# Optimization experiments

Hardware: AMD Instinct MI355X
Metric: run time of the kernel (lower is better)

The kernel has to match this reference:

```python
import jax, jax.numpy as jnp
import numpy as np

B, S, D = 2, 2048, 1024
H = 16
HD = D // H
MINUS_INFINITY = -1000000000.0


def setup_inputs() -> dict:
    key = jax.random.key(0)
    ks = jax.random.split(key, 6)
    sc = 0.02
    return {
        "x": jax.random.normal(ks[0], (B, S, D), dtype=jnp.float32),
        "Wq": jax.random.normal(ks[1], (D, D), dtype=jnp.float32) * sc,
        "Wk": jax.random.normal(ks[2], (D, D), dtype=jnp.float32) * sc,
        "Wv": jax.random.normal(ks[3], (D, D), dtype=jnp.float32) * sc,
        "Wo": jax.random.normal(ks[4], (D, D), dtype=jnp.float32) * sc,
        "bo": jnp.zeros((D,), dtype=jnp.float32),
    }


def reference(x, Wq, Wk, Wv, Wo, bo):
    b, n, _ = x.shape
    # Linear with transpose_b=True: x @ W.T
    q = jnp.einsum('bnd,ed->bne', x, Wq).reshape(b, n, H, HD).transpose(0, 2, 1, 3)
    k = jnp.einsum('bnd,ed->bne', x, Wk).reshape(b, n, H, HD).transpose(0, 2, 1, 3)
    v = jnp.einsum('bnd,ed->bne', x, Wv).reshape(b, n, H, HD).transpose(0, 2, 1, 3)
    scores = jnp.einsum('bhqd,bhkd->bhqk', q, k) * (1.0 / HD ** 0.5)
    mask = jnp.triu(jnp.ones((n, n), dtype=scores.dtype), k=1) * MINUS_INFINITY
    scores = scores + mask[None, None, :, :]
    attn = jax.nn.softmax(scores, axis=-1)  # dropout prob = 0.0
    ctx = jnp.einsum('bhqk,bhkd->bhqd', attn, v)
    ctx = ctx.transpose(0, 2, 1, 3).reshape(b, n, D)
    return jnp.einsum('bnd,ed->bne', ctx, Wo) + bo
```

## Files before the change

kernel.cpp:

```cpp
#include <hip/hip_runtime.h>
#include <hip/hip_bf16.h>

#define B_  2
#define S_  2048
#define D_  1024
#define H_  16
#define HD_ 64

typedef __attribute__((ext_vector_type(8))) short short8;
typedef __attribute__((ext_vector_type(4))) float f32x4;

__device__ __forceinline__ unsigned short f2b(float f) {
    __hip_bfloat16 h = __float2bfloat16(f);
    unsigned short u;
    __builtin_memcpy(&u, &h, 2);
    return u;
}

__device__ __forceinline__ float exp2_raw(float x) {
    float r;
    asm("v_exp_f32 %0, %1" : "=v"(r) : "v"(x));
    return r;
}

__device__ __forceinline__ unsigned int cvt_pk_bf16(float lo, float hi) {
    unsigned int r;
    asm("v_cvt_pk_bf16_f32 %0, %1, %2" : "=v"(r) : "v"(lo), "v"(hi));
    return r;
}

typedef __attribute__((address_space(1))) const unsigned int g_u32;
typedef __attribute__((address_space(3))) unsigned int l_u32;
__device__ __forceinline__ void gload_lds16(const void* g, void* l) {
    __builtin_amdgcn_global_load_lds((g_u32*)g, (l_u32*)l, 16, 0, 0);
}

__global__ __launch_bounds__(256) void convert_kernel(
    const float* __restrict__ x,  const float* __restrict__ Wq,
    const float* __restrict__ Wk, const float* __restrict__ Wv,
    const float* __restrict__ Wo, unsigned short* __restrict__ dst)
{
    const long long i4 = blockIdx.x * 256 + threadIdx.x;
    const long long e  = i4 * 4;
    const long long M1 = 1048576LL;
    const float* src;
    if      (e < 4 * M1) src = x  + e;
    else if (e < 5 * M1) src = Wq + (e - 4 * M1);
    else if (e < 6 * M1) src = Wk + (e - 5 * M1);
    else if (e < 7 * M1) src = Wv + (e - 6 * M1);
    else                 src = Wo + (e - 7 * M1);
    float4 v = *(const float4*)src;
    unsigned long long pk = (unsigned long long)f2b(v.x)
                          | ((unsigned long long)f2b(v.y) << 16)
                          | ((unsigned long long)f2b(v.z) << 32)
                          | ((unsigned long long)f2b(v.w) << 48);
    *(unsigned long long*)&dst[e] = pk;
}

__global__ __launch_bounds__(256) void qkv_proj_kernel(
    const unsigned short* __restrict__ x,
    const unsigned short* __restrict__ Wq,
    const unsigned short* __restrict__ Wk,
    const unsigned short* __restrict__ Wv,
    unsigned short* __restrict__ q_ws,
    unsigned short* __restrict__ k_ws,
    unsigned short* __restrict__ vT_ws)
{
    __shared__ unsigned short a_lds[2][128 * 32];
    __shared__ unsigned short b_lds[2][128 * 32];

    const int m0 = blockIdx.x * 128;
    const int n0 = blockIdx.y * 128;
    const int which = blockIdx.z;
    const unsigned short* W = (which == 0) ? Wq : (which == 1) ? Wk : Wv;

    const int tid  = threadIdx.x;
    const int wave = tid >> 6;
    const int lane = tid & 63;
    const int l15  = lane & 15;
    const int quad = lane >> 4;
    const int wm = (wave & 1) * 64;
    const int wn = (wave >> 1) * 64;

    const int srow = tid >> 2;
    const int scol = (tid & 3) * 8;
    const int soff = tid * 8;

    f32x4 acc[4][4];
    #pragma unroll
    for (int sm = 0; sm < 4; ++sm)
        #pragma unroll
        for (int sn = 0; sn < 4; ++sn)
            #pragma unroll
            for (int r = 0; r < 4; ++r) acc[sm][sn][r] = 0.f;

    #pragma unroll
    for (int p = 0; p < 2; ++p) {
        gload_lds16(&x[(m0 + srow + p * 64) * D_ + scol], &a_lds[0][p * 2048 + soff]);
        gload_lds16(&W[(n0 + srow + p * 64) * D_ + scol], &b_lds[0][p * 2048 + soff]);
    }
    __syncthreads();

    for (int t = 0; t < 32; ++t) {
        const int cur = t & 1;
        if (t < 31) {
            const int kk = (t + 1) * 32;
            #pragma unroll
            for (int p = 0; p < 2; ++p) {
                gload_lds16(&x[(m0 + srow + p * 64) * D_ + kk + scol],
                            &a_lds[cur ^ 1][p * 2048 + soff]);
                gload_lds16(&W[(n0 + srow + p * 64) * D_ + kk + scol],
                            &b_lds[cur ^ 1][p * 2048 + soff]);
            }
        }
        short8 af[4], bf[4];
        #pragma unroll
        for (int s = 0; s < 4; ++s) {
            af[s] = *(const short8*)&a_lds[cur][(wm + s * 16 + l15) * 32 + quad * 8];
            bf[s] = *(const short8*)&b_lds[cur][(wn + s * 16 + l15) * 32 + quad * 8];
        }
        #pragma unroll
        for (int sm = 0; sm < 4; ++sm)
            #pragma unroll
            for (int sn = 0; sn < 4; ++sn)
                acc[sm][sn] = __builtin_amdgcn_mfma_f32_16x16x32_bf16(
                    af[sm], bf[sn], acc[sm][sn], 0, 0, 0);
        __syncthreads();
    }

    #pragma unroll
    for (int sm = 0; sm < 4; ++sm) {
        #pragma unroll
        for (int sn = 0; sn < 4; ++sn) {
            const int n  = n0 + wn + sn * 16 + l15;
            const int h  = n >> 6;
            const int hd = n & 63;
            const int mbase = m0 + wm + sm * 16 + quad * 4;
            const int b     = mbase >> 11;
            const int sbase = mbase & 2047;
            if (which == 2) {
                unsigned long long pk =
                      (unsigned long long)cvt_pk_bf16(acc[sm][sn][0], acc[sm][sn][1])
                    | ((unsigned long long)cvt_pk_bf16(acc[sm][sn][2], acc[sm][sn][3]) << 32);
                *(unsigned long long*)&vT_ws[((b * H_ + h) * HD_ + hd) * S_ + sbase] = pk;
            } else if (which == 0) {
                #pragma unroll
                for (int r = 0; r < 4; ++r)
                    q_ws[((b * H_ + h) * S_ + (sbase + r)) * HD_ + hd] =
                        f2b(acc[sm][sn][r] * (0.125f * 1.44269504f));
            } else {
                #pragma unroll
                for (int r = 0; r < 4; ++r)
                    k_ws[((b * H_ + h) * S_ + (sbase + r)) * HD_ + hd] =
                        f2b(acc[sm][sn][r]);
            }
        }
    }
}

__global__ __launch_bounds__(256) void attn_kernel(
    const unsigned short* __restrict__ q_ws,
    const unsigned short* __restrict__ k_ws,
    const unsigned short* __restrict__ vT_ws,
    unsigned short* __restrict__ ctx_ws)
{
    __shared__ unsigned short k_lds[2 * 64 * 64];
    __shared__ unsigned short vT_lds[2 * 64 * 64];

    const int bh = blockIdx.x;
    const int qt = 31 - (int)blockIdx.y;

    const int tid  = threadIdx.x;
    const int wave = tid >> 6;
    const int lane = tid & 63;
    const int l15  = lane & 15;
    const int quad = lane >> 4;
    const int r0   = tid >> 3;
    const int c8   = tid & 7;

    const unsigned short* Qh = q_ws + bh * (S_ * HD_);
    const unsigned short* Kh = k_ws + bh * (S_ * HD_);
    const unsigned short* Vt = vT_ws + bh * (HD_ * S_);
    const int b = bh >> 4;
    const int h = bh & 15;

    const int src0 = l15 + 32 * (quad & 1);
    const int src1 = src0 + 16;
    const int sel  = quad >> 1;

    const int qg = qt * 64 + wave * 16 + l15;

    const int scol = (c8 ^ (r0 & 7)) * 8;
    const int d0 = r0 * 64 + c8 * 8;
    const int d1 = d0 + 2048;
    const int xr8 = (l15 & 7) << 3;

    gload_lds16(&Kh[r0 * HD_ + scol],        &k_lds[d0]);
    gload_lds16(&Kh[(r0 + 32) * HD_ + scol], &k_lds[d1]);
    gload_lds16(&Vt[r0 * S_ + scol],         &vT_lds[d0]);
    gload_lds16(&Vt[(r0 + 32) * S_ + scol],  &vT_lds[d1]);

    short8 aq[2];
    aq[0] = *(const short8*)&Qh[qg * HD_ + quad * 8];
    aq[1] = *(const short8*)&Qh[qg * HD_ + 32 + quad * 8];

    __syncthreads();

    float l_lane = 0.f;
    f32x4 o[4];
    #pragma unroll
    for (int f = 0; f < 4; ++f)
        #pragma unroll
        for (int r = 0; r < 4; ++r) o[f][r] = 0.f;

    for (int kt = 0; kt <= qt; ++kt) {
        const int cb = (kt & 1) * 4096;
        if (kt < qt) {
            const int nk0 = (kt + 1) * 64;
            const int nbb = 4096 - cb;
            gload_lds16(&Kh[(nk0 + r0) * HD_ + scol],      &k_lds[nbb + d0]);
            gload_lds16(&Kh[(nk0 + r0 + 32) * HD_ + scol], &k_lds[nbb + d1]);
            gload_lds16(&Vt[r0 * S_ + nk0 + scol],         &vT_lds[nbb + d0]);
            gload_lds16(&Vt[(r0 + 32) * S_ + nk0 + scol],  &vT_lds[nbb + d1]);
        }

        f32x4 sc[4];
        #pragma unroll
        for (int f = 0; f < 4; ++f)
            #pragma unroll
            for (int r = 0; r < 4; ++r) sc[f][r] = 0.f;
        #pragma unroll
        for (int f = 0; f < 4; ++f)
            #pragma unroll
            for (int kc = 0; kc < 2; ++kc) {
                short8 ak = *(const short8*)&k_lds[cb + (f * 16 + l15) * 64
                                                  + ((kc * 32 + quad * 8) ^ xr8)];
                sc[f] = __builtin_amdgcn_mfma_f32_16x16x32_bf16(ak, aq[kc], sc[f], 0, 0, 0);
            }

        float p[4][4];
        if (kt == qt) {
            const int kbase = kt * 64 + quad * 4;
            #pragma unroll
            for (int f = 0; f < 4; ++f)
                #pragma unroll
                for (int r = 0; r < 4; ++r) {
                    const float pv = exp2_raw(sc[f][r]);
                    p[f][r] = (kbase + f * 16 + r > qg) ? 0.f : pv;
                    l_lane += p[f][r];
                }
        } else {
            #pragma unroll
            for (int f = 0; f < 4; ++f)
                #pragma unroll
                for (int r = 0; r < 4; ++r) {
                    p[f][r] = exp2_raw(sc[f][r]);
                    l_lane += p[f][r];
                }
        }

        unsigned int pd[4][2];
        #pragma unroll
        for (int f = 0; f < 4; ++f) {
            pd[f][0] = cvt_pk_bf16(p[f][0], p[f][1]);
            pd[f][1] = cvt_pk_bf16(p[f][2], p[f][3]);
        }

        #pragma unroll
        for (int c = 0; c < 2; ++c) {
            const int a0 = __shfl((int)pd[c * 2][0],     src0, 64);
            const int a1 = __shfl((int)pd[c * 2][1],     src0, 64);
            const int a2 = __shfl((int)pd[c * 2][0],     src1, 64);
            const int a3 = __shfl((int)pd[c * 2][1],     src1, 64);
            const int b0 = __shfl((int)pd[c * 2 + 1][0], src0, 64);
            const int b1 = __shfl((int)pd[c * 2 + 1][1], src0, 64);
            const int b2 = __shfl((int)pd[c * 2 + 1][0], src1, 64);
            const int b3 = __shfl((int)pd[c * 2 + 1][1], src1, 64);
            union { int i[4]; short8 s; } u2;
            u2.i[0] = sel ? b0 : a0;
            u2.i[1] = sel ? b1 : a1;
            u2.i[2] = sel ? b2 : a2;
            u2.i[3] = sel ? b3 : a3;
            #pragma unroll
            for (int f = 0; f < 4; ++f) {
                short8 av = *(const short8*)&vT_lds[cb + (f * 16 + l15) * 64
                                                   + ((c * 32 + quad * 8) ^ xr8)];
                o[f] = __builtin_amdgcn_mfma_f32_16x16x32_bf16(av, u2.s, o[f], 0, 0, 0);
            }
        }

        __syncthreads();
    }

    float l = l_lane;
    l += __shfl_xor(l, 16, 64);
    l += __shfl_xor(l, 32, 64);
    const float inv_l = 1.0f / l;

    #pragma unroll
    for (int f = 0; f < 4; ++f) {
        unsigned long long pk =
              (unsigned long long)cvt_pk_bf16(o[f][0] * inv_l, o[f][1] * inv_l)
            | ((unsigned long long)cvt_pk_bf16(o[f][2] * inv_l, o[f][3] * inv_l) << 32);
        *(unsigned long long*)&ctx_ws[(b * S_ + qg) * D_ + h * 64 + f * 16 + quad * 4] = pk;
    }
}

__global__ __launch_bounds__(256) void out_proj_kernel(
    const unsigned short* __restrict__ ctx,
    const unsigned short* __restrict__ Wo,
    const float* __restrict__ bo,
    float* __restrict__ out)
{
    __shared__ unsigned short a_lds[2][128 * 32];
    __shared__ unsigned short b_lds[2][128 * 32];

    const int m0 = blockIdx.x * 128;
    const int n0 = blockIdx.y * 128;

    const int tid  = threadIdx.x;
    const int wave = tid >> 6;
    const int lane = tid & 63;
    const int l15  = lane & 15;
    const int quad = lane >> 4;
    const int wm = (wave & 1) * 64;
    const int wn = (wave >> 1) * 64;

    const int srow = tid >> 2;
    const int scol = (tid & 3) * 8;
    const int soff = tid * 8;

    f32x4 acc[4][4];
    #pragma unroll
    for (int sm = 0; sm < 4; ++sm)
        #pragma unroll
        for (int sn = 0; sn < 4; ++sn)
            #pragma unroll
            for (int r = 0; r < 4; ++r) acc[sm][sn][r] = 0.f;

    #pragma unroll
    for (int p = 0; p < 2; ++p) {
        gload_lds16(&ctx[(m0 + srow + p * 64) * D_ + scol], &a_lds[0][p * 2048 + soff]);
        gload_lds16(&Wo[(n0 + srow + p * 64) * D_ + scol],  &b_lds[0][p * 2048 + soff]);
    }
    __syncthreads();

    for (int t = 0; t < 32; ++t) {
        const int cur = t & 1;
        if (t < 31) {
            const int kk = (t + 1) * 32;
            #pragma unroll
            for (int p = 0; p < 2; ++p) {
                gload_lds16(&ctx[(m0 + srow + p * 64) * D_ + kk + scol],
                            &a_lds[cur ^ 1][p * 2048 + soff]);
                gload_lds16(&Wo[(n0 + srow + p * 64) * D_ + kk + scol],
                            &b_lds[cur ^ 1][p * 2048 + soff]);
            }
        }
        short8 af[4], bf[4];
        #pragma unroll
        for (int s = 0; s < 4; ++s) {
            af[s] = *(const short8*)&a_lds[cur][(wm + s * 16 + l15) * 32 + quad * 8];
            bf[s] = *(const short8*)&b_lds[cur][(wn + s * 16 + l15) * 32 + quad * 8];
        }
        #pragma unroll
        for (int sm = 0; sm < 4; ++sm)
            #pragma unroll
            for (int sn = 0; sn < 4; ++sn)
                acc[sm][sn] = __builtin_amdgcn_mfma_f32_16x16x32_bf16(
                    af[sm], bf[sn], acc[sm][sn], 0, 0, 0);
        __syncthreads();
    }

    #pragma unroll
    for (int sm = 0; sm < 4; ++sm) {
        #pragma unroll
        for (int sn = 0; sn < 4; ++sn) {
            const int n = n0 + wn + sn * 16 + l15;
            const float bias = bo[n];
            const int mbase = m0 + wm + sm * 16 + quad * 4;
            #pragma unroll
            for (int r = 0; r < 4; ++r)
                out[(mbase + r) * D_ + n] = acc[sm][sn][r] + bias;
        }
    }
}

extern "C" void kernel_launch(void* const* d_in, const int* in_sizes, int n_in,
                              void* d_out, int out_size, void* d_ws, size_t ws_size,
                              hipStream_t stream) {
    const float* x  = (const float*)d_in[0];
    const float* Wq = (const float*)d_in[1];
    const float* Wk = (const float*)d_in[2];
    const float* Wv = (const float*)d_in[3];
    const float* Wo = (const float*)d_in[4];
    const float* bo = (const float*)d_in[5];
    float* out = (float*)d_out;

    const size_t M1 = 1048576;
    const size_t SZ = 4 * M1;

    unsigned short* xb  = (unsigned short*)d_ws;
    unsigned short* wqb = xb  + SZ;
    unsigned short* wkb = wqb + M1;
    unsigned short* wvb = wkb + M1;
    unsigned short* wob = wvb + M1;
    unsigned short* q_ws   = wob + M1;
    unsigned short* k_ws   = q_ws + SZ;
    unsigned short* vT_ws  = k_ws + SZ;
    unsigned short* ctx_ws = vT_ws + SZ;

    convert_kernel<<<dim3(8192), 256, 0, stream>>>(x, Wq, Wk, Wv, Wo, xb);
    qkv_proj_kernel<<<dim3(32, 8, 3), 256, 0, stream>>>(xb, wqb, wkb, wvb, q_ws, k_ws, vT_ws);
    attn_kernel<<<dim3(32, 32), 256, 0, stream>>>(q_ws, k_ws, vT_ws, ctx_ws);
    out_proj_kernel<<<dim3(32, 8), 256, 0, stream>>>(ctx_ws, wob, bo, out);
}
```

Measured before the change: 191.6 us.

## Restructure attention into single-wave blocks reading K/V directly from global

Replaces the 4-wave, LDS double-buffered attention kernel with 2048 one-wave workgroups, each handling 32 query rows as two 16-row halves. K and V are loaded directly from global memory (relying on L2/cache) instead of being staged through LDS, and each loaded K/V fragment is reused across both query halves. The diagonal tile is specialised so the even half-tile skips unnecessary work. This removes LDS traffic and __syncthreads but gives up cross-wave sharing of K/V tiles, increasing global/L2 load volume and exposing load latency without explicit prefetch.

```diff
diff --git a/kernel.cpp b/kernel.cpp
--- a/kernel.cpp
+++ b/kernel.cpp
@@ -158,25 +158,115 @@
     }
 }
 
-__global__ __launch_bounds__(256) void attn_kernel(
+template<int FMAX, int CMAX, bool MASK>
+__device__ __forceinline__ void attn_tile(
+    const int k0,
+    const unsigned short* __restrict__ Kh,
+    const unsigned short* __restrict__ Vt,
+    const short8* aq0, const short8* aq1,
+    f32x4* o0, f32x4* o1, float& l0, float& l1,
+    const int l15, const int quad, const int qg0, const int qg1,
+    const int src0, const int src1, const int sel)
+{
+    short8 ak[FMAX][2];
+    #pragma unroll
+    for (int f = 0; f < FMAX; ++f)
+        #pragma unroll
+        for (int kc = 0; kc < 2; ++kc)
+            ak[f][kc] = *(const short8*)&Kh[(k0 + f * 16 + l15) * HD_ + kc * 32 + quad * 8];
+    short8 av[CMAX][4];
+    #pragma unroll
+    for (int c = 0; c < CMAX; ++c)
+        #pragma unroll
+        for (int f = 0; f < 4; ++f)
+            av[c][f] = *(const short8*)&Vt[(f * 16 + l15) * S_ + k0 + c * 32 + quad * 8];
+
+    f32x4 sc0[FMAX], sc1[FMAX];
+    #pragma unroll
+    for (int f = 0; f < FMAX; ++f)
+        #pragma unroll
+        for (int r = 0; r < 4; ++r) { sc0[f][r] = 0.f; sc1[f][r] = 0.f; }
+    #pragma unroll
+    for (int f = 0; f < FMAX; ++f)
+        #pragma unroll
+        for (int kc = 0; kc < 2; ++kc) {
+            sc0[f] = __builtin_amdgcn_mfma_f32_16x16x32_bf16(ak[f][kc], aq0[kc], sc0[f], 0, 0, 0);
+            sc1[f] = __builtin_amdgcn_mfma_f32_16x16x32_bf16(ak[f][kc], aq1[kc], sc1[f], 0, 0, 0);
+        }
+
+    float p0[FMAX][4], p1[FMAX][4];
+    #pragma unroll
+    for (int f = 0; f < FMAX; ++f)
+        #pragma unroll
+        for (int r = 0; r < 4; ++r) {
+            float v0 = exp2_raw(sc0[f][r]);
+            float v1 = exp2_raw(sc1[f][r]);
+            if (MASK) {
+                const int key = k0 + f * 16 + quad * 4 + r;
+                v0 = (key > qg0) ? 0.f : v0;
+                v1 = (key > qg1) ? 0.f : v1;
+            }
+            p0[f][r] = v0; l0 += v0;
+            p1[f][r] = v1; l1 += v1;
+        }
+
+    unsigned int pd0[FMAX][2], pd1[FMAX][2];
+    #pragma unroll
+    for (int f = 0; f < FMAX; ++f) {
+        pd0[f][0] = cvt_pk_bf16(p0[f][0], p0[f][1]);
+        pd0[f][1] = cvt_pk_bf16(p0[f][2], p0[f][3]);
+        pd1[f][0] = cvt_pk_bf16(p1[f][0], p1[f][1]);
+        pd1[f][1] = cvt_pk_bf16(p1[f][2], p1[f][3]);
+    }
+
+    #pragma unroll
+    for (int c = 0; c < CMAX; ++c) {
+        union { int i[4]; short8 s; } u20, u21;
+        {
+            const int a0 = __shfl((int)pd0[c * 2][0],     src0, 64);
+            const int a1 = __shfl((int)pd0[c * 2][1],     src0, 64);
+            const int a2 = __shfl((int)pd0[c * 2][0],     src1, 64);
+            const int a3 = __shfl((int)pd0[c * 2][1],     src1, 64);
+            const int b0 = __shfl((int)pd0[c * 2 + 1][0], src0, 64);
+            const int b1 = __shfl((int)pd0[c * 2 + 1][1], src0, 64);
+            const int b2 = __shfl((int)pd0[c * 2 + 1][0], src1, 64);
+            const int b3 = __shfl((int)pd0[c * 2 + 1][1], src1, 64);
+            u20.i[0] = sel ? b0 : a0;  u20.i[1] = sel ? b1 : a1;
+            u20.i[2] = sel ? b2 : a2;  u20.i[3] = sel ? b3 : a3;
+        }
+        {
+            const int a0 = __shfl((int)pd1[c * 2][0],     src0, 64);
+            const int a1 = __shfl((int)pd1[c * 2][1],     src0, 64);
+            const int a2 = __shfl((int)pd1[c * 2][0],     src1, 64);
+            const int a3 = __shfl((int)pd1[c * 2][1],     src1, 64);
+            const int b0 = __shfl((int)pd1[c * 2 + 1][0], src0, 64);
+            const int b1 = __shfl((int)pd1[c * 2 + 1][1], src0, 64);
+            const int b2 = __shfl((int)pd1[c * 2 + 1][0], src1, 64);
+            const int b3 = __shfl((int)pd1[c * 2 + 1][1], src1, 64);
+            u21.i[0] = sel ? b0 : a0;  u21.i[1] = sel ? b1 : a1;
+            u21.i[2] = sel ? b2 : a2;  u21.i[3] = sel ? b3 : a3;
+        }
+        #pragma unroll
+        for (int f = 0; f < 4; ++f) {
+            o0[f] = __builtin_amdgcn_mfma_f32_16x16x32_bf16(av[c][f], u20.s, o0[f], 0, 0, 0);
+            o1[f] = __builtin_amdgcn_mfma_f32_16x16x32_bf16(av[c][f], u21.s, o1[f], 0, 0, 0);
+        }
+    }
+}
+
+__global__ __launch_bounds__(64) void attn_kernel(
     const unsigned short* __restrict__ q_ws,
     const unsigned short* __restrict__ k_ws,
     const unsigned short* __restrict__ vT_ws,
     unsigned short* __restrict__ ctx_ws)
 {
-    __shared__ unsigned short k_lds[2 * 64 * 64];
-    __shared__ unsigned short vT_lds[2 * 64 * 64];
-
-    const int bh = blockIdx.x;
-    const int qt = 31 - (int)blockIdx.y;
-
-    const int tid  = threadIdx.x;
-    const int wave = tid >> 6;
-    const int lane = tid & 63;
+    const int wgid = blockIdx.x;
+    const int bh   = wgid & 31;
+    const int qsub = 63 - (wgid >> 5);
+
+    const int lane = threadIdx.x;
     const int l15  = lane & 15;
     const int quad = lane >> 4;
-    const int r0   = tid >> 3;
-    const int c8   = tid & 7;
 
     const unsigned short* Qh = q_ws + bh * (S_ * HD_);
     const unsigned short* Kh = k_ws + bh * (S_ * HD_);
@@ -188,121 +278,53 @@
     const int src1 = src0 + 16;
     const int sel  = quad >> 1;
 
-    const int qg = qt * 64 + wave * 16 + l15;
-
-    const int scol = (c8 ^ (r0 & 7)) * 8;
-    const int d0 = r0 * 64 + c8 * 8;
-    const int d1 = d0 + 2048;
-    const int xr8 = (l15 & 7) << 3;
-
-    gload_lds16(&Kh[r0 * HD_ + scol],        &k_lds[d0]);
-    gload_lds16(&Kh[(r0 + 32) * HD_ + scol], &k_lds[d1]);
-    gload_lds16(&Vt[r0 * S_ + scol],         &vT_lds[d0]);
-    gload_lds16(&Vt[(r0 + 32) * S_ + scol],  &vT_lds[d1]);
-
-    short8 aq[2];
-    aq[0] = *(const short8*)&Qh[qg * HD_ + quad * 8];
-    aq[1] = *(const short8*)&Qh[qg * HD_ + 32 + quad * 8];
-
-    __syncthreads();
-
-    float l_lane = 0.f;
-    f32x4 o[4];
+    const int q0  = qsub * 32;
+    const int qg0 = q0 + l15;
+    const int qg1 = q0 + 16 + l15;
+
+    short8 aq0[2], aq1[2];
+    aq0[0] = *(const short8*)&Qh[qg0 * HD_ + quad * 8];
+    aq0[1] = *(const short8*)&Qh[qg0 * HD_ + 32 + quad * 8];
+    aq1[0] = *(const short8*)&Qh[qg1 * HD_ + quad * 8];
+    aq1[1] = *(const short8*)&Qh[qg1 * HD_ + 32 + quad * 8];
+
+    float l0 = 0.f, l1 = 0.f;
+    f32x4 o0[4], o1[4];
     #pragma unroll
     for (int f = 0; f < 4; ++f)
         #pragma unroll
-        for (int r = 0; r < 4; ++r) o[f][r] = 0.f;
-
-    for (int kt = 0; kt <= qt; ++kt) {
-        const int cb = (kt & 1) * 4096;
-        if (kt < qt) {
-            const int nk0 = (kt + 1) * 64;
-            const int nbb = 4096 - cb;
-            gload_lds16(&Kh[(nk0 + r0) * HD_ + scol],      &k_lds[nbb + d0]);
-            gload_lds16(&Kh[(nk0 + r0 + 32) * HD_ + scol], &k_lds[nbb + d1]);
-            gload_lds16(&Vt[r0 * S_ + nk0 + scol],         &vT_lds[nbb + d0]);
-            gload_lds16(&Vt[(r0 + 32) * S_ + nk0 + scol],  &vT_lds[nbb + d1]);
-        }
-
-        f32x4 sc[4];
-        #pragma unroll
-        for (int f = 0; f < 4; ++f)
-            #pragma unroll
-            for (int r = 0; r < 4; ++r) sc[f][r] = 0.f;
-        #pragma unroll
-        for (int f = 0; f < 4; ++f)
-            #pragma unroll
-            for (int kc = 0; kc < 2; ++kc) {
-                short8 ak = *(const short8*)&k_lds[cb + (f * 16 + l15) * 64
-                                                  + ((kc * 32 + quad * 8) ^ xr8)];
-                sc[f] = __builtin_amdgcn_mfma_f32_16x16x32_bf16(ak, aq[kc], sc[f], 0, 0, 0);
-            }
-
-        float p[4][4];
-        if (kt == qt) {
-            const int kbase = kt * 64 + quad * 4;
-            #pragma unroll
-            for (int f = 0; f < 4; ++f)
-                #pragma unroll
-                for (int r = 0; r < 4; ++r) {
-                    const float pv = exp2_raw(sc[f][r]);
-                    p[f][r] = (kbase + f * 16 + r > qg) ? 0.f : pv;
-                    l_lane += p[f][r];
-                }
-        } else {
-            #pragma unroll
-            for (int f = 0; f < 4; ++f)
-                #pragma unroll
-                for (int r = 0; r < 4; ++r) {
-                    p[f][r] = exp2_raw(sc[f][r]);
-                    l_lane += p[f][r];
-                }
-        }
-
-        unsigned int pd[4][2];
-        #pragma unroll
-        for (int f = 0; f < 4; ++f) {
-            pd[f][0] = cvt_pk_bf16(p[f][0], p[f][1]);
-            pd[f][1] = cvt_pk_bf16(p[f][2], p[f][3]);
-        }
-
-        #pragma unroll
-        for (int c = 0; c < 2; ++c) {
-            const int a0 = __shfl((int)pd[c * 2][0],     src0, 64);
-            const int a1 = __shfl((int)pd[c * 2][1],     src0, 64);
-            const int a2 = __shfl((int)pd[c * 2][0],     src1, 64);
-            const int a3 = __shfl((int)pd[c * 2][1],     src1, 64);
-            const int b0 = __shfl((int)pd[c * 2 + 1][0], src0, 64);
-            const int b1 = __shfl((int)pd[c * 2 + 1][1], src0, 64);
-            const int b2 = __shfl((int)pd[c * 2 + 1][0], src1, 64);
-            const int b3 = __shfl((int)pd[c * 2 + 1][1], src1, 64);
-            union { int i[4]; short8 s; } u2;
-            u2.i[0] = sel ? b0 : a0;
-            u2.i[1] = sel ? b1 : a1;
-            u2.i[2] = sel ? b2 : a2;
-            u2.i[3] = sel ? b3 : a3;
-            #pragma unroll
-            for (int f = 0; f < 4; ++f) {
-                short8 av = *(const short8*)&vT_lds[cb + (f * 16 + l15) * 64
-                                                   + ((c * 32 + quad * 8) ^ xr8)];
-                o[f] = __builtin_amdgcn_mfma_f32_16x16x32_bf16(av, u2.s, o[f], 0, 0, 0);
-            }
-        }
-
-        __syncthreads();
-    }
-
-    float l = l_lane;
-    l += __shfl_xor(l, 16, 64);
-    l += __shfl_xor(l, 32, 64);
-    const float inv_l = 1.0f / l;
+        for (int r = 0; r < 4; ++r) { o0[f][r] = 0.f; o1[f][r] = 0.f; }
+
+    const int NT = (qsub >> 1) + 1;
+
+    for (int kt = 0; kt < NT - 1; ++kt)
+        attn_tile<4, 2, false>(kt * 64, Kh, Vt, aq0, aq1, o0, o1, l0, l1,
+                               l15, quad, qg0, qg1, src0, src1, sel);
+    const int k0 = (NT - 1) * 64;
+    if (qsub & 1)
+        attn_tile<4, 2, true>(k0, Kh, Vt, aq0, aq1, o0, o1, l0, l1,
+                              l15, quad, qg0, qg1, src0, src1, sel);
+    else
+        attn_tile<2, 1, true>(k0, Kh, Vt, aq0, aq1, o0, o1, l0, l1,
+                              l15, quad, qg0, qg1, src0, src1, sel);
+
+    l0 += __shfl_xor(l0, 16, 64);
+    l0 += __shfl_xor(l0, 32, 64);
+    l1 += __shfl_xor(l1, 16, 64);
+    l1 += __shfl_xor(l1, 32, 64);
+    const float inv0 = 1.0f / l0;
+    const float inv1 = 1.0f / l1;
 
     #pragma unroll
     for (int f = 0; f < 4; ++f) {
-        unsigned long long pk =
-              (unsigned long long)cvt_pk_bf16(o[f][0] * inv_l, o[f][1] * inv_l)
-            | ((unsigned long long)cvt_pk_bf16(o[f][2] * inv_l, o[f][3] * inv_l) << 32);
-        *(unsigned long long*)&ctx_ws[(b * S_ + qg) * D_ + h * 64 + f * 16 + quad * 4] = pk;
+        unsigned long long pk0 =
+              (unsigned long long)cvt_pk_bf16(o0[f][0] * inv0, o0[f][1] * inv0)
+            | ((unsigned long long)cvt_pk_bf16(o0[f][2] * inv0, o0[f][3] * inv0) << 32);
+        *(unsigned long long*)&ctx_ws[(b * S_ + qg0) * D_ + h * 64 + f * 16 + quad * 4] = pk0;
+        unsigned long long pk1 =
+              (unsigned long long)cvt_pk_bf16(o1[f][0] * inv1, o1[f][1] * inv1)
+            | ((unsigned long long)cvt_pk_bf16(o1[f][2] * inv1, o1[f][3] * inv1) << 32);
+        *(unsigned long long*)&ctx_ws[(b * S_ + qg1) * D_ + h * 64 + f * 16 + quad * 4] = pk1;
     }
 }
 
@@ -412,6 +434,6 @@
 
     convert_kernel<<<dim3(8192), 256, 0, stream>>>(x, Wq, Wk, Wv, Wo, xb);
     qkv_proj_kernel<<<dim3(32, 8, 3), 256, 0, stream>>>(xb, wqb, wkb, wvb, q_ws, k_ws, vT_ws);
-    attn_kernel<<<dim3(32, 32), 256, 0, stream>>>(q_ws, k_ws, vT_ws, ctx_ws);
+    attn_kernel<<<dim3(2048), 64, 0, stream>>>(q_ws, k_ws, vT_ws, ctx_ws);
     out_proj_kernel<<<dim3(32, 8), 256, 0, stream>>>(ctx_ws, wob, bo, out);
 }
```

Result: slower. 220.2 us (+14.9%).

## Fuse fp32-to-bf16 conversion into projection GEMM tile loads

Applied to the files above, without the earlier changes.

Removes the separate conversion kernel and has the QKV and output projection GEMMs read fp32 inputs and weights directly. The loaded values are converted to bf16 in registers and written into LDS, with the next tile's global loads issued before the MFMAs and the LDS stores placed after them. This avoids a kernel launch and the round trip of writing and re-reading bf16 copies. In exchange the GEMMs read twice as many bytes per tile, x is re-converted by every N-block, and the direct global-to-LDS async loads are replaced by register-staged loads that raise register pressure.

```diff
diff --git a/kernel.cpp b/kernel.cpp
--- a/kernel.cpp
+++ b/kernel.cpp
@@ -35,33 +35,11 @@
     __builtin_amdgcn_global_load_lds((g_u32*)g, (l_u32*)l, 16, 0, 0);
 }
 
-__global__ __launch_bounds__(256) void convert_kernel(
-    const float* __restrict__ x,  const float* __restrict__ Wq,
-    const float* __restrict__ Wk, const float* __restrict__ Wv,
-    const float* __restrict__ Wo, unsigned short* __restrict__ dst)
-{
-    const long long i4 = blockIdx.x * 256 + threadIdx.x;
-    const long long e  = i4 * 4;
-    const long long M1 = 1048576LL;
-    const float* src;
-    if      (e < 4 * M1) src = x  + e;
-    else if (e < 5 * M1) src = Wq + (e - 4 * M1);
-    else if (e < 6 * M1) src = Wk + (e - 5 * M1);
-    else if (e < 7 * M1) src = Wv + (e - 6 * M1);
-    else                 src = Wo + (e - 7 * M1);
-    float4 v = *(const float4*)src;
-    unsigned long long pk = (unsigned long long)f2b(v.x)
-                          | ((unsigned long long)f2b(v.y) << 16)
-                          | ((unsigned long long)f2b(v.z) << 32)
-                          | ((unsigned long long)f2b(v.w) << 48);
-    *(unsigned long long*)&dst[e] = pk;
-}
-
 __global__ __launch_bounds__(256) void qkv_proj_kernel(
-    const unsigned short* __restrict__ x,
-    const unsigned short* __restrict__ Wq,
-    const unsigned short* __restrict__ Wk,
-    const unsigned short* __restrict__ Wv,
+    const float* __restrict__ x,
+    const float* __restrict__ Wq,
+    const float* __restrict__ Wk,
+    const float* __restrict__ Wv,
     unsigned short* __restrict__ q_ws,
     unsigned short* __restrict__ k_ws,
     unsigned short* __restrict__ vT_ws)
@@ -72,7 +50,7 @@
     const int m0 = blockIdx.x * 128;
     const int n0 = blockIdx.y * 128;
     const int which = blockIdx.z;
-    const unsigned short* W = (which == 0) ? Wq : (which == 1) ? Wk : Wv;
+    const float* W = (which == 0) ? Wq : (which == 1) ? Wk : Wv;
 
     const int tid  = threadIdx.x;
     const int wave = tid >> 6;
@@ -82,10 +60,6 @@
     const int wm = (wave & 1) * 64;
     const int wn = (wave >> 1) * 64;
 
-    const int srow = tid >> 2;
-    const int scol = (tid & 3) * 8;
-    const int soff = tid * 8;
-
     f32x4 acc[4][4];
     #pragma unroll
     for (int sm = 0; sm < 4; ++sm)
@@ -95,22 +69,32 @@
             for (int r = 0; r < 4; ++r) acc[sm][sn][r] = 0.f;
 
     #pragma unroll
-    for (int p = 0; p < 2; ++p) {
-        gload_lds16(&x[(m0 + srow + p * 64) * D_ + scol], &a_lds[0][p * 2048 + soff]);
-        gload_lds16(&W[(n0 + srow + p * 64) * D_ + scol], &b_lds[0][p * 2048 + soff]);
+    for (int p = 0; p < 4; ++p) {
+        const int idx = p * 256 + tid;
+        const int row = idx >> 3;
+        const int c4  = (idx & 7) * 4;
+        float4 va = *(const float4*)&x[(m0 + row) * D_ + c4];
+        float4 vb = *(const float4*)&W[(n0 + row) * D_ + c4];
+        uint2 ua, ub;
+        ua.x = cvt_pk_bf16(va.x, va.y);  ua.y = cvt_pk_bf16(va.z, va.w);
+        ub.x = cvt_pk_bf16(vb.x, vb.y);  ub.y = cvt_pk_bf16(vb.z, vb.w);
+        *(uint2*)&a_lds[0][row * 32 + c4] = ua;
+        *(uint2*)&b_lds[0][row * 32 + c4] = ub;
     }
     __syncthreads();
 
     for (int t = 0; t < 32; ++t) {
         const int cur = t & 1;
+        float4 va[4], vb[4];
         if (t < 31) {
             const int kk = (t + 1) * 32;
             #pragma unroll
-            for (int p = 0; p < 2; ++p) {
-                gload_lds16(&x[(m0 + srow + p * 64) * D_ + kk + scol],
-                            &a_lds[cur ^ 1][p * 2048 + soff]);
-                gload_lds16(&W[(n0 + srow + p * 64) * D_ + kk + scol],
-                            &b_lds[cur ^ 1][p * 2048 + soff]);
+            for (int p = 0; p < 4; ++p) {
+                const int idx = p * 256 + tid;
+                const int row = idx >> 3;
+                const int c4  = (idx & 7) * 4;
+                va[p] = *(const float4*)&x[(m0 + row) * D_ + kk + c4];
+                vb[p] = *(const float4*)&W[(n0 + row) * D_ + kk + c4];
             }
         }
         short8 af[4], bf[4];
@@ -125,6 +109,19 @@
             for (int sn = 0; sn < 4; ++sn)
                 acc[sm][sn] = __builtin_amdgcn_mfma_f32_16x16x32_bf16(
                     af[sm], bf[sn], acc[sm][sn], 0, 0, 0);
+        if (t < 31) {
+            #pragma unroll
+            for (int p = 0; p < 4; ++p) {
+                const int idx = p * 256 + tid;
+                const int row = idx >> 3;
+                const int c4  = (idx & 7) * 4;
+                uint2 ua, ub;
+                ua.x = cvt_pk_bf16(va[p].x, va[p].y);  ua.y = cvt_pk_bf16(va[p].z, va[p].w);
+                ub.x = cvt_pk_bf16(vb[p].x, vb[p].y);  ub.y = cvt_pk_bf16(vb[p].z, vb[p].w);
+                *(uint2*)&a_lds[cur ^ 1][row * 32 + c4] = ua;
+                *(uint2*)&b_lds[cur ^ 1][row * 32 + c4] = ub;
+            }
+        }
         __syncthreads();
     }
 
@@ -308,7 +305,7 @@
 
 __global__ __launch_bounds__(256) void out_proj_kernel(
     const unsigned short* __restrict__ ctx,
-    const unsigned short* __restrict__ Wo,
+    const float* __restrict__ Wo,
     const float* __restrict__ bo,
     float* __restrict__ out)
 {
@@ -339,22 +336,35 @@
             for (int r = 0; r < 4; ++r) acc[sm][sn][r] = 0.f;
 
     #pragma unroll
-    for (int p = 0; p < 2; ++p) {
+    for (int p = 0; p < 2; ++p)
         gload_lds16(&ctx[(m0 + srow + p * 64) * D_ + scol], &a_lds[0][p * 2048 + soff]);
-        gload_lds16(&Wo[(n0 + srow + p * 64) * D_ + scol],  &b_lds[0][p * 2048 + soff]);
+    #pragma unroll
+    for (int p = 0; p < 4; ++p) {
+        const int idx = p * 256 + tid;
+        const int row = idx >> 3;
+        const int c4  = (idx & 7) * 4;
+        float4 vb = *(const float4*)&Wo[(n0 + row) * D_ + c4];
+        uint2 ub;
+        ub.x = cvt_pk_bf16(vb.x, vb.y);  ub.y = cvt_pk_bf16(vb.z, vb.w);
+        *(uint2*)&b_lds[0][row * 32 + c4] = ub;
     }
     __syncthreads();
 
     for (int t = 0; t < 32; ++t) {
         const int cur = t & 1;
+        float4 vb[4];
         if (t < 31) {
             const int kk = (t + 1) * 32;
             #pragma unroll
-            for (int p = 0; p < 2; ++p) {
+            for (int p = 0; p < 2; ++p)
                 gload_lds16(&ctx[(m0 + srow + p * 64) * D_ + kk + scol],
                             &a_lds[cur ^ 1][p * 2048 + soff]);
-                gload_lds16(&Wo[(n0 + srow + p * 64) * D_ + kk + scol],
-                            &b_lds[cur ^ 1][p * 2048 + soff]);
+            #pragma unroll
+            for (int p = 0; p < 4; ++p) {
+                const int idx = p * 256 + tid;
+                const int row = idx >> 3;
+                const int c4  = (idx & 7) * 4;
+                vb[p] = *(const float4*)&Wo[(n0 + row) * D_ + kk + c4];
             }
         }
         short8 af[4], bf[4];
@@ -369,6 +379,17 @@
             for (int sn = 0; sn < 4; ++sn)
                 acc[sm][sn] = __builtin_amdgcn_mfma_f32_16x16x32_bf16(
                     af[sm], bf[sn], acc[sm][sn], 0, 0, 0);
+        if (t < 31) {
+            #pragma unroll
+            for (int p = 0; p < 4; ++p) {
+                const int idx = p * 256 + tid;
+                const int row = idx >> 3;
+                const int c4  = (idx & 7) * 4;
+                uint2 ub;
+                ub.x = cvt_pk_bf16(vb[p].x, vb[p].y);  ub.y = cvt_pk_bf16(vb[p].z, vb[p].w);
+                *(uint2*)&b_lds[cur ^ 1][row * 32 + c4] = ub;
+            }
+        }
         __syncthreads();
     }
 
@@ -400,18 +421,12 @@
     const size_t M1 = 1048576;
     const size_t SZ = 4 * M1;
 
-    unsigned short* xb  = (unsigned short*)d_ws;
-    unsigned short* wqb = xb  + SZ;
-    unsigned short* wkb = wqb + M1;
-    unsigned short* wvb = wkb + M1;
-    unsigned short* wob = wvb + M1;
-    unsigned short* q_ws   = wob + M1;
+    unsigned short* q_ws   = (unsigned short*)d_ws;
     unsigned short* k_ws   = q_ws + SZ;
     unsigned short* vT_ws  = k_ws + SZ;
     unsigned short* ctx_ws = vT_ws + SZ;
 
-    convert_kernel<<<dim3(8192), 256, 0, stream>>>(x, Wq, Wk, Wv, Wo, xb);
-    qkv_proj_kernel<<<dim3(32, 8, 3), 256, 0, stream>>>(xb, wqb, wkb, wvb, q_ws, k_ws, vT_ws);
+    qkv_proj_kernel<<<dim3(32, 8, 3), 256, 0, stream>>>(x, Wq, Wk, Wv, q_ws, k_ws, vT_ws);
     attn_kernel<<<dim3(32, 32), 256, 0, stream>>>(q_ws, k_ws, vT_ws, ctx_ws);
-    out_proj_kernel<<<dim3(32, 8), 256, 0, stream>>>(ctx_ws, wob, bo, out);
-}
+    out_proj_kernel<<<dim3(32, 8), 256, 0, stream>>>(ctx_ws, Wo, bo, out);
+}
```

Result: slower. 209.6 us (+9.4%).
